# Kernel optimization log

Measured on AMD Instinct MI355X. Metric: run time of the kernel, lower is better.

## Reference

```python
import jax, jax.numpy as jnp
import numpy as np

N_EMBD = 1024
N_HEAD = 16
BLOCK_SIZE = 2048
HEAD_DIM = N_EMBD // N_HEAD
NEG_INF = -1e10


def precompute_rotary_emb(dim, max_positions):
    positions = jnp.arange(max_positions, dtype=jnp.float32)
    freqs = 1.0 / 10000.0 ** (jnp.arange(0, dim, 2, dtype=jnp.float32) / dim)
    t_theta = jnp.outer(positions, freqs)  # (max_positions, dim//2)
    return jnp.stack([jnp.cos(t_theta), jnp.sin(t_theta)], axis=-1)  # (P, dim//2, 2)


def setup_inputs() -> dict:
    key = jax.random.key(0)
    ks = jax.random.split(key, 9)
    s = 1.0 / np.sqrt(N_EMBD)
    x = jax.random.normal(ks[0], (2, 2048, N_EMBD), dtype=jnp.float32)
    Wq = jax.random.uniform(ks[1], (N_EMBD, N_EMBD), minval=-s, maxval=s)
    bq = jax.random.uniform(ks[2], (N_EMBD,), minval=-s, maxval=s)
    Wk = jax.random.uniform(ks[3], (N_EMBD, N_EMBD), minval=-s, maxval=s)
    bk = jax.random.uniform(ks[4], (N_EMBD,), minval=-s, maxval=s)
    Wv = jax.random.uniform(ks[5], (N_EMBD, N_EMBD), minval=-s, maxval=s)
    bv = jax.random.uniform(ks[6], (N_EMBD,), minval=-s, maxval=s)
    Wp = jax.random.uniform(ks[7], (N_EMBD, N_EMBD), minval=-s, maxval=s)
    bp = jax.random.uniform(ks[8], (N_EMBD,), minval=-s, maxval=s)
    rope_cache = precompute_rotary_emb(HEAD_DIM, BLOCK_SIZE)
    return {"x": x, "Wq": Wq, "bq": bq, "Wk": Wk, "bk": bk,
            "Wv": Wv, "bv": bv, "Wp": Wp, "bp": bp, "rope_cache": rope_cache}


def _apply_rope(t, rope_cache, T):
    # t: (B, T, H, hd); rope applied per-head, vectorized over H
    B, _, H, hd = t.shape
    cos = rope_cache[:T, :, 0][None, :, None, :]  # (1, T, 1, hd//2)
    sin = rope_cache[:T, :, 1][None, :, None, :]
    tr = t.reshape(B, T, H, hd // 2, 2)
    real = tr[..., 0] * cos - tr[..., 1] * sin
    imag = tr[..., 0] * sin + tr[..., 1] * cos
    return jnp.stack([real, imag], axis=-1).reshape(B, T, H, hd)


def reference(x, Wq, bq, Wk, bk, Wv, bv, Wp, bp, rope_cache):
    B, T, C = x.shape
    H, hd = N_HEAD, C // N_HEAD
    q = (x @ Wq.T + bq).reshape(B, T, H, hd)
    k = (x @ Wk.T + bk).reshape(B, T, H, hd)
    v = (x @ Wv.T + bv).reshape(B, T, H, hd)
    q = _apply_rope(q, rope_cache, T)
    k = _apply_rope(k, rope_cache, T)
    # (B, H, T, T)
    att = jnp.einsum('bthd,bshd->bhts', q, k) / jnp.sqrt(jnp.float32(hd))
    causal = jnp.tril(jnp.ones((T, T), dtype=bool))
    att = jnp.where(causal[None, None], att, NEG_INF)
    att = jax.nn.softmax(att, axis=-1)
    y = jnp.einsum('bhts,bshd->bthd', att, v).reshape(B, T, C)
    return y @ Wp.T + bp
```

## Files before the change

### kernel.cpp

```cpp
#include <hip/hip_runtime.h>
#include <hip/hip_bf16.h>
#include <stdint.h>

#define N_EMBD 1024
#define T_SEQ  2048
#define NB     2
#define NH     16
#define HD     64
#define BTROWS (NB*T_SEQ)

typedef __attribute__((ext_vector_type(8))) short s16x8;
typedef __attribute__((ext_vector_type(4))) float f32x4;

__device__ __forceinline__ unsigned short f2bf(float f) {
    union { float f; unsigned int u; } c; c.f = f;
    unsigned int u = c.u;
    unsigned int r = (u + 0x7fffu + ((u >> 16) & 1u)) >> 16;
    return (unsigned short)r;
}

__device__ __forceinline__ unsigned int pack2bf(float a, float b) {
    __hip_bfloat162 h = __float22bfloat162_rn(make_float2(a, b));
    union { __hip_bfloat162 h; unsigned int u; } c; c.h = h;
    return c.u;
}

#define GLDS16(gsrc, ldst) \
  __builtin_amdgcn_global_load_lds((const __attribute__((address_space(1))) unsigned int*)(gsrc), \
                                   (__attribute__((address_space(3))) unsigned int*)(ldst), 16, 0, 0)

__global__ void cast_all(const float* __restrict__ x,  const float* __restrict__ wq,
                         const float* __restrict__ wk, const float* __restrict__ wv,
                         const float* __restrict__ wp, unsigned short* __restrict__ dst) {
    const int i = blockIdx.x * 256 + threadIdx.x;
    const float* src; int off;
    if (i < 1048576) { src = x; off = i; }
    else {
        const int j = i - 1048576;
        const int w = j >> 18;
        off = j & 262143;
        src = (w == 0) ? wq : (w == 1) ? wk : (w == 2) ? wv : wp;
    }
    float4 v = reinterpret_cast<const float4*>(src)[off];
    ushort4 o;
    o.x = f2bf(v.x); o.y = f2bf(v.y); o.z = f2bf(v.z); o.w = f2bf(v.w);
    reinterpret_cast<ushort4*>(dst)[i] = o;
}

__global__ __launch_bounds__(256)
void gemm_qkv(const unsigned short* __restrict__ A,
              const unsigned short* __restrict__ Wb,
              const float* __restrict__ bq, const float* __restrict__ bk, const float* __restrict__ bv,
              unsigned short* __restrict__ Ob,
              const float* __restrict__ rope)
{
    constexpr int K = 1024, N = 1024;
    const int z = blockIdx.z;
    const unsigned short* Bt = Wb + (size_t)z * 1048576;
    const float* bias = (z == 0) ? bq : (z == 1) ? bk : bv;
    unsigned short* outp = Ob + (size_t)z * 4194304;
    const bool dorope = (z < 2);

    __shared__ unsigned short Al[128*32];
    __shared__ unsigned short Bl[128*32];
    const int tid = threadIdx.x;
    const int w = tid >> 6, l = tid & 63;
    const int bm = blockIdx.x * 128;
    const int bn = blockIdx.y * 128;
    const int wr = (w >> 1) * 64, wc = (w & 1) * 64;
    const int lr = l & 15, lg = l >> 4;
    const int scol = (l & 3) * 8;
    const int srow_in = l >> 2;

    f32x4 acc[4][4] = {};

    for (int k0 = 0; k0 < K; k0 += 32) {
        #pragma unroll
        for (int j = 0; j < 2; ++j) {
            const int i = w*2 + j;
            const int row = i*16 + srow_in;
            GLDS16(A  + (size_t)(bm+row)*K + k0 + scol, Al + i*512);
            GLDS16(Bt + (size_t)(bn+row)*K + k0 + scol, Bl + i*512);
        }
        __syncthreads();
        s16x8 af[4], bfv[4];
        #pragma unroll
        for (int m = 0; m < 4; ++m)
            af[m] = *(const s16x8*)(Al + (wr + m*16 + lr)*32 + lg*8);
        #pragma unroll
        for (int n = 0; n < 4; ++n)
            bfv[n] = *(const s16x8*)(Bl + (wc + n*16 + lr)*32 + lg*8);
        #pragma unroll
        for (int m = 0; m < 4; ++m)
            #pragma unroll
            for (int n = 0; n < 4; ++n)
                acc[m][n] = __builtin_amdgcn_mfma_f32_16x16x32_bf16(af[m], bfv[n], acc[m][n], 0, 0, 0);
        __syncthreads();
    }

    #pragma unroll
    for (int m = 0; m < 4; ++m) {
        const int row0 = bm + wr + m*16 + lg*4;
        #pragma unroll
        for (int n = 0; n < 4; ++n) {
            const int colg = bn + wc + n*16 + lr;
            const float bb = bias[colg];
            #pragma unroll
            for (int r = 0; r < 4; ++r) {
                const float val = acc[m][n][r] + bb;
                const int bt = row0 + r;
                float res = val;
                if (dorope) {
                    const float pairv = __shfl_xor(val, 1);
                    const int t = bt & (T_SEQ-1);
                    const int d = colg & (HD-1);
                    const float2 cs = *(const float2*)(rope + (size_t)t*HD + (d >> 1)*2);
                    res = (d & 1) ? fmaf(pairv, cs.y,  val*cs.x)
                                  : fmaf(-pairv, cs.y, val*cs.x);
                }
                const int b_ = bt >> 11, h = colg >> 6, d2 = colg & (HD-1);
                outp[(((size_t)(b_*NH + h))*T_SEQ + (bt & (T_SEQ-1)))*HD + d2] = f2bf(res);
            }
        }
    }
}

__global__ __launch_bounds__(256)
void gemm_proj(const unsigned short* __restrict__ A,
               const unsigned short* __restrict__ Bt,
               const float* __restrict__ bias,
               float* __restrict__ outp)
{
    constexpr int K = 1024, N = 1024;
    __shared__ unsigned short Al[128*32];
    __shared__ unsigned short Bl[128*32];
    const int tid = threadIdx.x;
    const int w = tid >> 6, l = tid & 63;
    const int bm = blockIdx.x * 128;
    const int bn = blockIdx.y * 128;
    const int wr = (w >> 1) * 64, wc = (w & 1) * 64;
    const int lr = l & 15, lg = l >> 4;
    const int scol = (l & 3) * 8;
    const int srow_in = l >> 2;

    f32x4 acc[4][4] = {};

    for (int k0 = 0; k0 < K; k0 += 32) {
        #pragma unroll
        for (int j = 0; j < 2; ++j) {
            const int i = w*2 + j;
            const int row = i*16 + srow_in;
            GLDS16(A  + (size_t)(bm+row)*K + k0 + scol, Al + i*512);
            GLDS16(Bt + (size_t)(bn+row)*K + k0 + scol, Bl + i*512);
        }
        __syncthreads();
        s16x8 af[4], bfv[4];
        #pragma unroll
        for (int m = 0; m < 4; ++m)
            af[m] = *(const s16x8*)(Al + (wr + m*16 + lr)*32 + lg*8);
        #pragma unroll
        for (int n = 0; n < 4; ++n)
            bfv[n] = *(const s16x8*)(Bl + (wc + n*16 + lr)*32 + lg*8);
        #pragma unroll
        for (int m = 0; m < 4; ++m)
            #pragma unroll
            for (int n = 0; n < 4; ++n)
                acc[m][n] = __builtin_amdgcn_mfma_f32_16x16x32_bf16(af[m], bfv[n], acc[m][n], 0, 0, 0);
        __syncthreads();
    }

    #pragma unroll
    for (int m = 0; m < 4; ++m) {
        const int row0 = bm + wr + m*16 + lg*4;
        #pragma unroll
        for (int n = 0; n < 4; ++n) {
            const int colg = bn + wc + n*16 + lr;
            const float bb = bias[colg];
            #pragma unroll
            for (int r = 0; r < 4; ++r)
                outp[(size_t)(row0 + r)*N + colg] = acc[m][n][r] + bb;
        }
    }
}

__global__ __launch_bounds__(512)
void flash2(const unsigned short* __restrict__ Qg, const unsigned short* __restrict__ Kg,
            const unsigned short* __restrict__ Vg, unsigned short* __restrict__ Y)
{
    __shared__ unsigned short Kl[2][64*64];
    __shared__ unsigned short Vt[2][64*80];

    const int tid = threadIdx.x, w = tid >> 6, l = tid & 63;
    const int lr = l & 15, lg = l >> 4;
    const int bh = blockIdx.x & 31;
    const int pr = blockIdx.x >> 5;
    const int b_ = bh >> 4, h = bh & (NH-1);

    const unsigned short* Qb = Qg + (size_t)bh*T_SEQ*HD;
    const unsigned short* Kb = Kg + (size_t)bh*T_SEQ*HD;
    const unsigned short* Vb = Vg + (size_t)bh*T_SEQ*HD;

    const int krow  = tid >> 3;
    const int kloff = (tid & 7) ^ (krow & 7);
    const int vd0   = (tid & 7) * 8;
    const int vsig  = ((krow >> 5)) * 32 + ((krow >> 2) & 3) * 8 + ((krow >> 4) & 1) * 4 + (krow & 3);

    for (int side = 0; side < 2; ++side) {
        const int qb = side ? pr : (15 - pr);
        const int nt = 2*qb + 2;
        const int q0 = qb * 128;
        const int qrow = q0 + w*16 + lr;

        s16x8 qf[2];
        #pragma unroll
        for (int kk = 0; kk < 2; ++kk)
            qf[kk] = *(const s16x8*)(Qb + (size_t)(q0 + w*16 + lr)*HD + kk*32 + lg*8);

        f32x4 oacc[4] = {};
        float mrun = -3.0e38f, lrun = 0.0f;

        GLDS16(Kb + ((size_t)(0*64 + krow))*HD + kloff*8, &Kl[0][(w*64)*8]);
        {
            uint4 v0 = *(const uint4*)(Vb + ((size_t)krow)*HD + vd0);
            const unsigned short* pv = (const unsigned short*)&v0;
            #pragma unroll
            for (int e = 0; e < 8; ++e) Vt[0][(vd0 + e)*80 + vsig] = pv[e];
        }
        __syncthreads();

        int cur = 0;
        for (int t = 0; t < nt; ++t) {
            uint4 vnext;
            const bool pf = (t + 1 < nt);
            if (pf) {
                GLDS16(Kb + ((size_t)((t+1)*64 + krow))*HD + kloff*8, &Kl[cur^1][(w*64)*8]);
                vnext = *(const uint4*)(Vb + ((size_t)((t+1)*64 + krow))*HD + vd0);
            }

            f32x4 sac[4] = {};
            __builtin_amdgcn_s_setprio(1);
            #pragma unroll
            for (int kkd = 0; kkd < 2; ++kkd) {
                const int off = ((kkd*64 + lg*16) ^ ((lr & 7) << 4)) >> 1;
                #pragma unroll
                for (int m = 0; m < 4; ++m) {
                    s16x8 kf = *(const s16x8*)&Kl[cur][(m*16 + lr)*64 + off];
                    sac[m] = __builtin_amdgcn_mfma_f32_16x16x32_bf16(kf, qf[kkd], sac[m], 0, 0, 0);
                }
            }
            __builtin_amdgcn_s_setprio(0);

            float p[4][4];
            float pm = -3.0e38f;
            #pragma unroll
            for (int m = 0; m < 4; ++m)
                #pragma unroll
                for (int r = 0; r < 4; ++r) {
                    float s = sac[m][r] * 0.125f;
                    if (t*64 + m*16 + lg*4 + r > qrow) s = -1e10f;
                    p[m][r] = s;
                    pm = fmaxf(pm, s);
                }
            pm = fmaxf(pm, __shfl_xor(pm, 16));
            pm = fmaxf(pm, __shfl_xor(pm, 32));
            const float mnew = fmaxf(mrun, pm);
            const float corr = __expf(mrun - mnew);
            mrun = mnew;
            float ls = 0.0f;
            #pragma unroll
            for (int m = 0; m < 4; ++m)
                #pragma unroll
                for (int r = 0; r < 4; ++r) {
                    const float e = __expf(p[m][r] - mnew);
                    p[m][r] = e;
                    ls += e;
                }
            ls += __shfl_xor(ls, 16);
            ls += __shfl_xor(ls, 32);
            lrun = lrun * corr + ls;

            float corrv[4];
            #pragma unroll
            for (int r = 0; r < 4; ++r) corrv[r] = __shfl(corr, lg*4 + r);
            #pragma unroll
            for (int n = 0; n < 4; ++n)
                #pragma unroll
                for (int r = 0; r < 4; ++r) oacc[n][r] *= corrv[r];

            __builtin_amdgcn_s_setprio(1);
            #pragma unroll
            for (int kk2 = 0; kk2 < 2; ++kk2) {
                union { s16x8 v; unsigned int u[4]; } pa;
                pa.u[0] = pack2bf(p[2*kk2][0],   p[2*kk2][1]);
                pa.u[1] = pack2bf(p[2*kk2][2],   p[2*kk2][3]);
                pa.u[2] = pack2bf(p[2*kk2+1][0], p[2*kk2+1][1]);
                pa.u[3] = pack2bf(p[2*kk2+1][2], p[2*kk2+1][3]);
                #pragma unroll
                for (int n = 0; n < 4; ++n) {
                    s16x8 vf = *(const s16x8*)&Vt[cur][(n*16 + lr)*80 + kk2*32 + lg*8];
                    oacc[n] = __builtin_amdgcn_mfma_f32_16x16x32_bf16(pa.v, vf, oacc[n], 0, 0, 0);
                }
            }
            __builtin_amdgcn_s_setprio(0);

            if (pf) {
                const unsigned short* pv = (const unsigned short*)&vnext;
                #pragma unroll
                for (int e = 0; e < 8; ++e) Vt[cur^1][(vd0 + e)*80 + vsig] = pv[e];
            }
            __syncthreads();
            cur ^= 1;
        }

        const float inv = 1.0f / lrun;
        float invv[4];
        #pragma unroll
        for (int r = 0; r < 4; ++r) invv[r] = __shfl(inv, lg*4 + r);
        #pragma unroll
        for (int r = 0; r < 4; ++r) {
            const size_t base = ((size_t)(b_*T_SEQ + q0 + w*16 + lg*4 + r))*N_EMBD + h*HD;
            #pragma unroll
            for (int n = 0; n < 4; ++n)
                Y[base + n*16 + lr] = f2bf(oacc[n][r] * invv[r]);
        }
    }
}

#define MB(x) ((size_t)(x) << 20)

extern "C" void kernel_launch(void* const* d_in, const int* in_sizes, int n_in,
                              void* d_out, int out_size, void* d_ws, size_t ws_size,
                              hipStream_t stream) {
    const float* x    = (const float*)d_in[0];
    const float* Wq   = (const float*)d_in[1];
    const float* bq   = (const float*)d_in[2];
    const float* Wk   = (const float*)d_in[3];
    const float* bk   = (const float*)d_in[4];
    const float* Wv   = (const float*)d_in[5];
    const float* bv   = (const float*)d_in[6];
    const float* Wp   = (const float*)d_in[7];
    const float* bp   = (const float*)d_in[8];
    const float* rope = (const float*)d_in[9];

    char* ws = (char*)d_ws;
    unsigned short* xb  = (unsigned short*)(ws + MB(0));
    unsigned short* Wqb = (unsigned short*)(ws + MB(8));
    unsigned short* Wpb = (unsigned short*)(ws + MB(14));
    unsigned short* Qa  = (unsigned short*)(ws + MB(16));
    unsigned short* Ka  = (unsigned short*)(ws + MB(24));
    unsigned short* Va  = (unsigned short*)(ws + MB(32));
    unsigned short* y2  = (unsigned short*)(ws + MB(40));

    cast_all<<<8192, 256, 0, stream>>>(x, Wq, Wk, Wv, Wp, xb);

    gemm_qkv<<<dim3(BTROWS/128, N_EMBD/128, 3), 256, 0, stream>>>(xb, Wqb, bq, bk, bv, Qa, rope);

    flash2<<<256, 512, 0, stream>>>(Qa, Ka, Va, y2);

    gemm_proj<<<dim3(BTROWS/128, N_EMBD/128), 256, 0, stream>>>(y2, Wpb, bp, (float*)d_out);
}
```

Baseline: 223.7 us.

## Store V transposed from QKV GEMM and restructure flash attention with lazy rescaling

The QKV GEMM now writes V in a (head, dim, token) transposed layout with vectorized stores, so the attention kernel can load V tiles straight into shared memory with global_load_lds instead of scattering it through registers. The attention kernel moves from 512-thread blocks covering two 128-row query blocks to 256-thread blocks covering one 64-row query block each, over 1024 blocks, and applies the causal mask only on the diagonal tile. It also skips the running-max update and output rescale when the new max stays within a threshold of the old one. Finer blocks change how the causal work is balanced and raise the block count. The deferred rescale saves exp and multiply work but lets exponentials grow to about e^8 before renormalizing.

```diff
diff --git a/kernel.cpp b/kernel.cpp
--- a/kernel.cpp
+++ b/kernel.cpp
@@ -10,6 +10,7 @@
 #define BTROWS (NB*T_SEQ)
 
 typedef __attribute__((ext_vector_type(8))) short s16x8;
+typedef __attribute__((ext_vector_type(4))) short s16x4;
 typedef __attribute__((ext_vector_type(4))) float f32x4;
 
 __device__ __forceinline__ unsigned short f2bf(float f) {
@@ -105,21 +106,29 @@
         for (int n = 0; n < 4; ++n) {
             const int colg = bn + wc + n*16 + lr;
             const float bb = bias[colg];
-            #pragma unroll
-            for (int r = 0; r < 4; ++r) {
-                const float val = acc[m][n][r] + bb;
-                const int bt = row0 + r;
-                float res = val;
-                if (dorope) {
+            if (z == 2) {
+                const int h = colg >> 6, d2 = colg & (HD-1);
+                const int b_ = row0 >> 11, t0 = row0 & (T_SEQ-1);
+                ushort4 st;
+                st.x = f2bf(acc[m][n][0] + bb);
+                st.y = f2bf(acc[m][n][1] + bb);
+                st.z = f2bf(acc[m][n][2] + bb);
+                st.w = f2bf(acc[m][n][3] + bb);
+                *(ushort4*)(outp + ((size_t)(b_*NH + h)*HD + d2)*T_SEQ + t0) = st;
+            } else {
+                #pragma unroll
+                for (int r = 0; r < 4; ++r) {
+                    const float val = acc[m][n][r] + bb;
+                    const int bt = row0 + r;
                     const float pairv = __shfl_xor(val, 1);
                     const int t = bt & (T_SEQ-1);
                     const int d = colg & (HD-1);
                     const float2 cs = *(const float2*)(rope + (size_t)t*HD + (d >> 1)*2);
-                    res = (d & 1) ? fmaf(pairv, cs.y,  val*cs.x)
-                                  : fmaf(-pairv, cs.y, val*cs.x);
+                    const float res = (d & 1) ? fmaf(pairv, cs.y,  val*cs.x)
+                                              : fmaf(-pairv, cs.y, val*cs.x);
+                    const int b_ = bt >> 11, h = colg >> 6, d2 = colg & (HD-1);
+                    outp[(((size_t)(b_*NH + h))*T_SEQ + t)*HD + d2] = f2bf(res);
                 }
-                const int b_ = bt >> 11, h = colg >> 6, d2 = colg & (HD-1);
-                outp[(((size_t)(b_*NH + h))*T_SEQ + (bt & (T_SEQ-1)))*HD + d2] = f2bf(res);
             }
         }
     }
@@ -183,102 +192,105 @@
     }
 }
 
-__global__ __launch_bounds__(512)
-void flash2(const unsigned short* __restrict__ Qg, const unsigned short* __restrict__ Kg,
-            const unsigned short* __restrict__ Vg, unsigned short* __restrict__ Y)
+__global__ __launch_bounds__(256)
+void flash4(const unsigned short* __restrict__ Qg, const unsigned short* __restrict__ Kg,
+            const unsigned short* __restrict__ VTg, unsigned short* __restrict__ Y)
 {
-    __shared__ unsigned short Kl[2][64*64];
-    __shared__ unsigned short Vt[2][64*80];
+    __shared__ unsigned short Kl[2][4096];
+    __shared__ unsigned short Vl[2][4096];
 
     const int tid = threadIdx.x, w = tid >> 6, l = tid & 63;
     const int lr = l & 15, lg = l >> 4;
-    const int bh = blockIdx.x & 31;
-    const int pr = blockIdx.x >> 5;
-    const int b_ = bh >> 4, h = bh & (NH-1);
-
-    const unsigned short* Qb = Qg + (size_t)bh*T_SEQ*HD;
-    const unsigned short* Kb = Kg + (size_t)bh*T_SEQ*HD;
-    const unsigned short* Vb = Vg + (size_t)bh*T_SEQ*HD;
-
-    const int krow  = tid >> 3;
-    const int kloff = (tid & 7) ^ (krow & 7);
-    const int vd0   = (tid & 7) * 8;
-    const int vsig  = ((krow >> 5)) * 32 + ((krow >> 2) & 3) * 8 + ((krow >> 4) & 1) * 4 + (krow & 3);
-
-    for (int side = 0; side < 2; ++side) {
-        const int qb = side ? pr : (15 - pr);
-        const int nt = 2*qb + 2;
-        const int q0 = qb * 128;
-        const int qrow = q0 + w*16 + lr;
-
-        s16x8 qf[2];
-        #pragma unroll
-        for (int kk = 0; kk < 2; ++kk)
-            qf[kk] = *(const s16x8*)(Qb + (size_t)(q0 + w*16 + lr)*HD + kk*32 + lg*8);
-
-        f32x4 oacc[4] = {};
-        float mrun = -3.0e38f, lrun = 0.0f;
-
-        GLDS16(Kb + ((size_t)(0*64 + krow))*HD + kloff*8, &Kl[0][(w*64)*8]);
-        {
-            uint4 v0 = *(const uint4*)(Vb + ((size_t)krow)*HD + vd0);
-            const unsigned short* pv = (const unsigned short*)&v0;
-            #pragma unroll
-            for (int e = 0; e < 8; ++e) Vt[0][(vd0 + e)*80 + vsig] = pv[e];
-        }
-        __syncthreads();
-
-        int cur = 0;
-        for (int t = 0; t < nt; ++t) {
-            uint4 vnext;
-            const bool pf = (t + 1 < nt);
-            if (pf) {
-                GLDS16(Kb + ((size_t)((t+1)*64 + krow))*HD + kloff*8, &Kl[cur^1][(w*64)*8]);
-                vnext = *(const uint4*)(Vb + ((size_t)((t+1)*64 + krow))*HD + vd0);
-            }
-
-            f32x4 sac[4] = {};
-            __builtin_amdgcn_s_setprio(1);
-            #pragma unroll
-            for (int kkd = 0; kkd < 2; ++kkd) {
-                const int off = ((kkd*64 + lg*16) ^ ((lr & 7) << 4)) >> 1;
-                #pragma unroll
-                for (int m = 0; m < 4; ++m) {
-                    s16x8 kf = *(const s16x8*)&Kl[cur][(m*16 + lr)*64 + off];
-                    sac[m] = __builtin_amdgcn_mfma_f32_16x16x32_bf16(kf, qf[kkd], sac[m], 0, 0, 0);
-                }
-            }
-            __builtin_amdgcn_s_setprio(0);
-
-            float p[4][4];
-            float pm = -3.0e38f;
-            #pragma unroll
-            for (int m = 0; m < 4; ++m)
-                #pragma unroll
-                for (int r = 0; r < 4; ++r) {
-                    float s = sac[m][r] * 0.125f;
-                    if (t*64 + m*16 + lg*4 + r > qrow) s = -1e10f;
-                    p[m][r] = s;
-                    pm = fmaxf(pm, s);
-                }
-            pm = fmaxf(pm, __shfl_xor(pm, 16));
-            pm = fmaxf(pm, __shfl_xor(pm, 32));
-            const float mnew = fmaxf(mrun, pm);
+    const int u = blockIdx.x >> 5, bh = blockIdx.x & 31;
+    const int qb = (u < 16) ? (31 - u) : (u - 16);
+    const int b_ = bh >> 4, hh = bh & (NH-1);
+
+    const unsigned short* Qb = Qg  + (size_t)bh*T_SEQ*HD;
+    const unsigned short* Kb = Kg  + (size_t)bh*T_SEQ*HD;
+    const unsigned short* Vb = VTg + (size_t)bh*HD*T_SEQ;
+
+    int soK[2], soV[2];
+    #pragma unroll
+    for (int i = 0; i < 2; ++i) {
+        const int p = i*256 + tid;
+        const int row = p >> 3, ps = p & 7;
+        soK[i] = row*HD    + ((ps ^ (row & 7))*8);
+        soV[i] = row*T_SEQ + ((ps ^ (row & 7))*8);
+    }
+
+    const int q0 = qb*64;
+    const int nt = qb + 1;
+    const int qrow = q0 + w*16 + lr;
+
+    s16x8 qf[2];
+    #pragma unroll
+    for (int kk = 0; kk < 2; ++kk)
+        qf[kk] = *(const s16x8*)(Qb + (size_t)qrow*HD + kk*32 + lg*8);
+
+    f32x4 oacc[4] = {};
+    float mrun = -3.0e38f, lrun = 0.0f;
+
+    #pragma unroll
+    for (int i = 0; i < 2; ++i) {
+        GLDS16(Kb + soK[i], &Kl[0][(i*256 + w*64)*8]);
+        GLDS16(Vb + soV[i], &Vl[0][(i*256 + w*64)*8]);
+    }
+    __syncthreads();
+
+    int cur = 0;
+    for (int t = 0; t < nt; ++t) {
+        if (t + 1 < nt) {
+            #pragma unroll
+            for (int i = 0; i < 2; ++i) {
+                GLDS16(Kb + (size_t)(t+1)*64*HD + soK[i], &Kl[cur^1][(i*256 + w*64)*8]);
+                GLDS16(Vb + (size_t)(t+1)*64    + soV[i], &Vl[cur^1][(i*256 + w*64)*8]);
+            }
+        }
+
+        f32x4 sac[4] = {};
+        __builtin_amdgcn_s_setprio(1);
+        #pragma unroll
+        for (int kkd = 0; kkd < 2; ++kkd) {
+            const int off = ((kkd*4 + lg) ^ (lr & 7)) * 8;
+            #pragma unroll
+            for (int n = 0; n < 4; ++n) {
+                s16x8 kf = *(const s16x8*)&Kl[cur][(n*16 + lr)*64 + off];
+                sac[n] = __builtin_amdgcn_mfma_f32_16x16x32_bf16(kf, qf[kkd], sac[n], 0, 0, 0);
+            }
+        }
+        __builtin_amdgcn_s_setprio(0);
+
+        float p[4][4];
+        float pm = -3.0e38f;
+        const bool maskt = (t == qb);
+        #pragma unroll
+        for (int n = 0; n < 4; ++n)
+            #pragma unroll
+            for (int r = 0; r < 4; ++r) {
+                float s = sac[n][r] * 0.125f;
+                if (maskt && (t*64 + n*16 + lg*4 + r > qrow)) s = -1e10f;
+                p[n][r] = s;
+                pm = fmaxf(pm, s);
+            }
+        pm = fmaxf(pm, __shfl_xor(pm, 16));
+        pm = fmaxf(pm, __shfl_xor(pm, 32));
+        const bool defer = __all(pm <= mrun + 8.0f) != 0;
+        const float mnew = defer ? mrun : fmaxf(mrun, pm);
+        float ls = 0.0f;
+        #pragma unroll
+        for (int n = 0; n < 4; ++n)
+            #pragma unroll
+            for (int r = 0; r < 4; ++r) {
+                const float e = __expf(p[n][r] - mnew);
+                p[n][r] = e;
+                ls += e;
+            }
+        ls += __shfl_xor(ls, 16);
+        ls += __shfl_xor(ls, 32);
+        if (!defer) {
             const float corr = __expf(mrun - mnew);
             mrun = mnew;
-            float ls = 0.0f;
-            #pragma unroll
-            for (int m = 0; m < 4; ++m)
-                #pragma unroll
-                for (int r = 0; r < 4; ++r) {
-                    const float e = __expf(p[m][r] - mnew);
-                    p[m][r] = e;
-                    ls += e;
-                }
-            ls += __shfl_xor(ls, 16);
-            ls += __shfl_xor(ls, 32);
             lrun = lrun * corr + ls;
-
             float corrv[4];
             #pragma unroll
             for (int r = 0; r < 4; ++r) corrv[r] = __shfl(corr, lg*4 + r);
@@ -286,43 +298,46 @@
             for (int n = 0; n < 4; ++n)
                 #pragma unroll
                 for (int r = 0; r < 4; ++r) oacc[n][r] *= corrv[r];
-
-            __builtin_amdgcn_s_setprio(1);
-            #pragma unroll
-            for (int kk2 = 0; kk2 < 2; ++kk2) {
-                union { s16x8 v; unsigned int u[4]; } pa;
-                pa.u[0] = pack2bf(p[2*kk2][0],   p[2*kk2][1]);
-                pa.u[1] = pack2bf(p[2*kk2][2],   p[2*kk2][3]);
-                pa.u[2] = pack2bf(p[2*kk2+1][0], p[2*kk2+1][1]);
-                pa.u[3] = pack2bf(p[2*kk2+1][2], p[2*kk2+1][3]);
-                #pragma unroll
-                for (int n = 0; n < 4; ++n) {
-                    s16x8 vf = *(const s16x8*)&Vt[cur][(n*16 + lr)*80 + kk2*32 + lg*8];
-                    oacc[n] = __builtin_amdgcn_mfma_f32_16x16x32_bf16(pa.v, vf, oacc[n], 0, 0, 0);
-                }
-            }
-            __builtin_amdgcn_s_setprio(0);
-
-            if (pf) {
-                const unsigned short* pv = (const unsigned short*)&vnext;
-                #pragma unroll
-                for (int e = 0; e < 8; ++e) Vt[cur^1][(vd0 + e)*80 + vsig] = pv[e];
-            }
-            __syncthreads();
-            cur ^= 1;
-        }
-
-        const float inv = 1.0f / lrun;
-        float invv[4];
-        #pragma unroll
-        for (int r = 0; r < 4; ++r) invv[r] = __shfl(inv, lg*4 + r);
-        #pragma unroll
-        for (int r = 0; r < 4; ++r) {
-            const size_t base = ((size_t)(b_*T_SEQ + q0 + w*16 + lg*4 + r))*N_EMBD + h*HD;
-            #pragma unroll
-            for (int n = 0; n < 4; ++n)
-                Y[base + n*16 + lr] = f2bf(oacc[n][r] * invv[r]);
-        }
+        } else {
+            lrun += ls;
+        }
+
+        __builtin_amdgcn_s_setprio(1);
+        #pragma unroll
+        for (int kk2 = 0; kk2 < 2; ++kk2) {
+            union { s16x8 v; unsigned uu[4]; } pa;
+            pa.uu[0] = pack2bf(p[2*kk2][0],   p[2*kk2][1]);
+            pa.uu[1] = pack2bf(p[2*kk2][2],   p[2*kk2][3]);
+            pa.uu[2] = pack2bf(p[2*kk2+1][0], p[2*kk2+1][1]);
+            pa.uu[3] = pack2bf(p[2*kk2+1][2], p[2*kk2+1][3]);
+            #pragma unroll
+            for (int n = 0; n < 4; ++n) {
+                const int d = n*16 + lr;
+                const int c0 = (4*kk2     + (lg >> 1)) ^ (lr & 7);
+                const int c1 = (4*kk2 + 2 + (lg >> 1)) ^ (lr & 7);
+                union { s16x8 v; s16x4 q[2]; } vf;
+                vf.q[0] = *(const s16x4*)&Vl[cur][d*64 + c0*8 + (lg & 1)*4];
+                vf.q[1] = *(const s16x4*)&Vl[cur][d*64 + c1*8 + (lg & 1)*4];
+                oacc[n] = __builtin_amdgcn_mfma_f32_16x16x32_bf16(pa.v, vf.v, oacc[n], 0, 0, 0);
+            }
+        }
+        __builtin_amdgcn_s_setprio(0);
+
+        __syncthreads();
+        cur ^= 1;
+    }
+
+    const float linv = 1.0f / lrun;
+    float invv[4];
+    #pragma unroll
+    for (int r = 0; r < 4; ++r) invv[r] = __shfl(linv, lg*4 + r);
+    #pragma unroll
+    for (int r = 0; r < 4; ++r) {
+        const int tq = q0 + w*16 + lg*4 + r;
+        const size_t base = ((size_t)(b_*T_SEQ + tq))*N_EMBD + hh*HD;
+        #pragma unroll
+        for (int n = 0; n < 4; ++n)
+            Y[base + n*16 + lr] = f2bf(oacc[n][r] * invv[r]);
     }
 }
 
@@ -347,15 +362,13 @@
     unsigned short* Wqb = (unsigned short*)(ws + MB(8));
     unsigned short* Wpb = (unsigned short*)(ws + MB(14));
     unsigned short* Qa  = (unsigned short*)(ws + MB(16));
-    unsigned short* Ka  = (unsigned short*)(ws + MB(24));
-    unsigned short* Va  = (unsigned short*)(ws + MB(32));
     unsigned short* y2  = (unsigned short*)(ws + MB(40));
 
     cast_all<<<8192, 256, 0, stream>>>(x, Wq, Wk, Wv, Wp, xb);
 
     gemm_qkv<<<dim3(BTROWS/128, N_EMBD/128, 3), 256, 0, stream>>>(xb, Wqb, bq, bk, bv, Qa, rope);
 
-    flash2<<<256, 512, 0, stream>>>(Qa, Ka, Va, y2);
+    flash4<<<1024, 256, 0, stream>>>(Qa, Qa + 4194304, Qa + 8388608, y2);
 
     gemm_proj<<<dim3(BTROWS/128, N_EMBD/128), 256, 0, stream>>>(y2, Wpb, bp, (float*)d_out);
 }
```

After: 213.9 us. -4.4%, faster.
